# Kernel optimization log

Measured on AMD Instinct MI355X. Metric: run time of the kernel, lower is better.

Reference implementation:

```python
import jax, jax.numpy as jnp
import numpy as np
from jax import lax

N = 2048
P = 256
F_J = 0.05      # sparsity of recurrent matrix J
F_OUT = 0.05    # sparsity of readout
DT = 0.1
ON_TIME = 10
T = 200


def _activation(x):
    # Tanh_shifted_and_scaled: rates in [0, 1]
    return 0.5 * (1.0 + jnp.tanh(x))


def setup_inputs() -> dict:
    key = jax.random.key(0)
    k1, k2, k3, k4, k5 = jax.random.split(key, 5)
    # patterns ~ Uniform(-1, 1), shape [N, P]
    patterns = jax.random.uniform(k1, (N, P), jnp.float32, -1.0, 1.0)
    # sparse recurrent matrix J: gaussian values, density F_J, gain g
    g = 10.0 * 0.1 ** 0.25 / np.sqrt(N * P * np.sqrt(F_J))
    J_dense = jax.random.normal(k2, (N, N), jnp.float32) * jnp.float32(g)
    mask = jax.random.uniform(k3, (N, N)) < F_J
    J = jnp.where(mask, J_dense, 0.0).astype(jnp.float32)
    # sparse readout: ones at a random F_OUT fraction of units (frozen)
    w_out = (jax.random.uniform(k4, (N,)) < F_OUT).astype(jnp.float32)
    return {"patterns": patterns, "J": J, "w_out": w_out, "N_time_steps": T}


def reference(patterns, J, w_out, N_time_steps):
    # Batched over all P patterns at once (columns of [N, P] state).
    n = patterns.shape[0]
    x0 = jnp.zeros_like(patterns)           # [N, P]
    r0 = _activation(x0)

    def step(carry, ti):
        x, rates = carry
        inp = jnp.where(ti < ON_TIME, patterns, 0.0)      # [N, P]
        x = x + DT * (-x + J @ rates + inp)               # [N, P]
        rates = _activation(x)
        out_t = w_out @ rates                             # [P]
        return (x, rates), out_t

    _, outs = lax.scan(step, (x0, r0), jnp.arange(N_time_steps))  # [T, P]
    readout = outs.T / n                                   # [P, T]
    return readout
```

## Files before the change

### kernel.cpp

```cpp
#include <hip/hip_runtime.h>
#include <hip/hip_bf16.h>


#define NN 2048
#define PP 256
#define DT_C 0.1f
#define ON_TIME_C 10

typedef __attribute__((ext_vector_type(8))) short bf16x8;
typedef __attribute__((ext_vector_type(4))) float f32x4;

__device__ __forceinline__ unsigned short bf16rne(float f) {
    unsigned b = __float_as_uint(f);
    return (unsigned short)((b + 0x7FFFu + ((b >> 16) & 1u)) >> 16);
}
__device__ __forceinline__ int kperm(int s) {
    return ((s & 15) >> 2) * 8 + (s & 3) + ((s >> 4) << 2);
}

__global__ void convert_J_kernel(const float* __restrict__ J,
                                 unsigned short* __restrict__ Jp) {
    int i = blockIdx.x * blockDim.x + threadIdx.x;
    int row = i >> 11, k = i & 2047;
    Jp[((size_t)row << 11) + (k & ~31) + kperm(k & 31)] = bf16rne(J[i]);
}

__global__ void init_kernel(float* __restrict__ x,
                            unsigned short* __restrict__ rT,
                            float* __restrict__ out, int nout) {
    int i = blockIdx.x * blockDim.x + threadIdx.x;
    x[i] = 0.0f;
    rT[i] = 0x3F00;
    if (i < nout) out[i] = 0.0f;
}

#define AS1 __attribute__((address_space(1)))
#define AS3 __attribute__((address_space(3)))
#define GLOAD16(g, l) \
    __builtin_amdgcn_global_load_lds((const AS1 void*)(g), (AS3 void*)(l), 16, 0, 0)

__global__ __launch_bounds__(256, 1) void gemm_step_kernel(
    const unsigned short* __restrict__ Jp,
    const unsigned short* __restrict__ rin,
    unsigned short* __restrict__ rout,
    float* __restrict__ x, const float* __restrict__ patterns,
    const float* __restrict__ w_out, float* __restrict__ out,
    int t, int T, int with_input) {

    __shared__ char smem[49152];

    const int tid  = threadIdx.x;
    const int w    = tid >> 6;
    const int lane = tid & 63;
    const int wm   = w >> 1, wn = w & 1;

    const int bid   = (blockIdx.x & 7) * 32 + (blockIdx.x >> 3);
    const int mbase = (bid >> 3) * 64;
    const int nbase = (bid & 7) * 32;

    const int r8 = lane >> 3, p8 = lane & 7;
    const int xr16 = (p8 ^ r8) * 16;
    const char* gA0 = (const char*)Jp  + (((size_t)(mbase + (2*w+0)*8 + r8)) << 12) + xr16;
    const char* gA1 = (const char*)Jp  + (((size_t)(mbase + (2*w+1)*8 + r8)) << 12) + xr16;
    const char* gB  = (const char*)rin + (((size_t)(nbase +  w*8      + r8)) << 12) + xr16;
    const int ldsA0 = (2*w+0) * 1024, ldsA1 = (2*w+1) * 1024, ldsB = 8192 + w * 1024;

    const int cx  = ((lane >> 4) ^ (lane & 7)) * 16;
    const int vA0 = (wm*32      + (lane & 15)) * 128 + cx;
    const int vA1 = (wm*32 + 16 + (lane & 15)) * 128 + cx;
    const int vB  = 8192 + (wn*16 + (lane & 15)) * 128 + cx;

    float xv[2][4], pat[2][4], wsc[2][4];
    #pragma unroll
    for (int mf = 0; mf < 2; ++mf)
        #pragma unroll
        for (int rg = 0; rg < 4; ++rg) {
            int m = mbase + wm*32 + mf*16 + 4*(lane>>4) + rg;
            int n = nbase + wn*16 + (lane & 15);
            size_t o = ((size_t)m << 8) + n;
            xv[mf][rg]  = x[o];
            pat[mf][rg] = with_input ? patterns[o] : 0.0f;
            wsc[mf][rg] = (w_out[m] != 0.0f) ? (1.0f / (float)NN) : 0.0f;
        }

    f32x4 acc[2] = {{0.f,0.f,0.f,0.f}, {0.f,0.f,0.f,0.f}};

    GLOAD16(gA0,       smem + 0*12288 + ldsA0);
    GLOAD16(gA1,       smem + 0*12288 + ldsA1);
    GLOAD16(gB,        smem + 0*12288 + ldsB);
    GLOAD16(gA0 + 128, smem + 1*12288 + ldsA0);
    GLOAD16(gA1 + 128, smem + 1*12288 + ldsA1);
    GLOAD16(gB  + 128, smem + 1*12288 + ldsB);

    #pragma unroll
    for (int ks = 0; ks < 32; ++ks) {
        if (ks < 30) {
            const int bo = ((ks + 2) & 3) * 12288;
            GLOAD16(gA0 + (ks+2)*128, smem + bo + ldsA0);
            GLOAD16(gA1 + (ks+2)*128, smem + bo + ldsA1);
            GLOAD16(gB  + (ks+2)*128, smem + bo + ldsB);
        }
        if (ks < 30)       asm volatile("s_waitcnt vmcnt(6)" ::: "memory");
        else if (ks == 30) asm volatile("s_waitcnt vmcnt(3)" ::: "memory");
        else               asm volatile("s_waitcnt vmcnt(0)" ::: "memory");
        __builtin_amdgcn_s_barrier();
        __builtin_amdgcn_sched_barrier(0);

        const int bb = (ks & 3) * 12288;
        bf16x8 a0  = *(const bf16x8*)(smem + bb + vA0);
        bf16x8 a1  = *(const bf16x8*)(smem + bb + vA1);
        bf16x8 b0  = *(const bf16x8*)(smem + bb + vB);
        bf16x8 a0h = *(const bf16x8*)(smem + bb + (vA0 ^ 64));
        bf16x8 a1h = *(const bf16x8*)(smem + bb + (vA1 ^ 64));
        bf16x8 b0h = *(const bf16x8*)(smem + bb + (vB  ^ 64));
        acc[0] = __builtin_amdgcn_mfma_f32_16x16x32_bf16(a0,  b0,  acc[0], 0, 0, 0);
        acc[1] = __builtin_amdgcn_mfma_f32_16x16x32_bf16(a1,  b0,  acc[1], 0, 0, 0);
        acc[0] = __builtin_amdgcn_mfma_f32_16x16x32_bf16(a0h, b0h, acc[0], 0, 0, 0);
        acc[1] = __builtin_amdgcn_mfma_f32_16x16x32_bf16(a1h, b0h, acc[1], 0, 0, 0);
    }

    __syncthreads();

    #pragma unroll
    for (int mf = 0; mf < 2; ++mf)
        #pragma unroll
        for (int rg = 0; rg < 4; ++rg) {
            float xo = xv[mf][rg];
            float xn = xo + DT_C * (acc[mf][rg] + pat[mf][rg] - xo);
            int m = mbase + wm*32 + mf*16 + 4*(lane>>4) + rg;
            int n = nbase + wn*16 + (lane & 15);
            x[((size_t)m << 8) + n] = xn;
            float r = 0.5f * (1.0f + tanhf(xn));
            if (wsc[mf][rg] != 0.0f)
                atomicAdd(&out[(size_t)n * T + t], r * wsc[mf][rg]);
            int mloc = wm*32 + mf*16 + 4*(lane>>4) + rg;
            int pos  = (mloc & 32) + kperm(mloc & 31);
            int nloc = wn*16 + (lane & 15);
            int byte = nloc*128 + (((pos >> 3) ^ (nloc & 7)) * 16) + (pos & 7)*2;
            *(unsigned short*)(smem + byte) = bf16rne(r);
        }
    __syncthreads();
    {
        int nl = tid >> 3, p = tid & 7;
        uint4 v = *(const uint4*)(smem + nl*128 + ((p ^ (nl & 7)) * 16));
        *(uint4*)((char*)rout + (((size_t)(nbase + nl)) << 12) + mbase*2 + p*16) = v;
    }
}

extern "C" void kernel_launch(void* const* d_in, const int* in_sizes, int n_in,
                              void* d_out, int out_size, void* d_ws, size_t ws_size,
                              hipStream_t stream) {
    const float* patterns = (const float*)d_in[0];
    const float* J        = (const float*)d_in[1];
    const float* w_out    = (const float*)d_in[2];
    float* out            = (float*)d_out;

    int T = out_size / PP;

    size_t off = 0;
    auto alloc = [&](size_t bytes) {
        void* p = (char*)d_ws + off;
        off += (bytes + 255) & ~(size_t)255;
        return p;
    };
    unsigned short* Jp = (unsigned short*)alloc((size_t)NN * NN * 2);
    unsigned short* r0 = (unsigned short*)alloc((size_t)PP * NN * 2);
    unsigned short* r1 = (unsigned short*)alloc((size_t)PP * NN * 2);
    float*          x  = (float*)         alloc((size_t)NN * PP * 4);
    (void)ws_size; (void)n_in; (void)in_sizes;

    convert_J_kernel<<<(NN * NN) / 256, 256, 0, stream>>>(J, Jp);
    init_kernel<<<(NN * PP) / 256, 256, 0, stream>>>(x, r0, out, PP * T);

    for (int t = 0; t < T; ++t) {
        const unsigned short* rin = (t & 1) ? r1 : r0;
        unsigned short*      rout = (t & 1) ? r0 : r1;
        gemm_step_kernel<<<256, 256, 0, stream>>>(Jp, rin, rout, x, patterns,
                                                  w_out, out, t, T,
                                                  (t < ON_TIME_C) ? 1 : 0);
    }
}
```

Baseline: 2.120 ms.

## Use 512-thread blocks with 128-wide K stages and one MFMA tile per wave

Doubles the block to 8 waves, so each wave now computes a single 16x16 output tile instead of two, and doubles the K chunk per pipeline stage to 128 (four MFMAs per stage, half as many barriers). LDS staging grows to 96 KB with a new 16-chunk XOR swizzle. The goal is more waves per CU to hide load latency and fewer barrier round trips per step. In exchange, each wave has fewer MFMAs to cover its LDS reads, and the large LDS footprint caps residency at one block per CU.

```diff
diff --git a/kernel.cpp b/kernel.cpp
--- a/kernel.cpp
+++ b/kernel.cpp
@@ -39,7 +39,7 @@
 #define GLOAD16(g, l) \
     __builtin_amdgcn_global_load_lds((const AS1 void*)(g), (AS3 void*)(l), 16, 0, 0)
 
-__global__ __launch_bounds__(256, 1) void gemm_step_kernel(
+__global__ __launch_bounds__(512, 1) void gemm_step_kernel(
     const unsigned short* __restrict__ Jp,
     const unsigned short* __restrict__ rin,
     unsigned short* __restrict__ rout,
@@ -47,7 +47,7 @@
     const float* __restrict__ w_out, float* __restrict__ out,
     int t, int T, int with_input) {
 
-    __shared__ char smem[49152];
+    __shared__ char smem[98304];
 
     const int tid  = threadIdx.x;
     const int w    = tid >> 6;
@@ -58,92 +58,91 @@
     const int mbase = (bid >> 3) * 64;
     const int nbase = (bid & 7) * 32;
 
-    const int r8 = lane >> 3, p8 = lane & 7;
-    const int xr16 = (p8 ^ r8) * 16;
-    const char* gA0 = (const char*)Jp  + (((size_t)(mbase + (2*w+0)*8 + r8)) << 12) + xr16;
-    const char* gA1 = (const char*)Jp  + (((size_t)(mbase + (2*w+1)*8 + r8)) << 12) + xr16;
-    const char* gB  = (const char*)rin + (((size_t)(nbase +  w*8      + r8)) << 12) + xr16;
-    const int ldsA0 = (2*w+0) * 1024, ldsA1 = (2*w+1) * 1024, ldsB = 8192 + w * 1024;
+    const int rA0 = 8 * w + (lane >> 4);
+    const int rA1 = rA0 + 4;
+    const int rB  = 4 * w + (lane >> 4);
+    const char* gA0 = (const char*)Jp  + (((size_t)(mbase + rA0)) << 12)
+                      + (((lane & 15) ^ (rA0 & 15)) << 4);
+    const char* gA1 = (const char*)Jp  + (((size_t)(mbase + rA1)) << 12)
+                      + (((lane & 15) ^ (rA1 & 15)) << 4);
+    const char* gB  = (const char*)rin + (((size_t)(nbase + rB )) << 12)
+                      + (((lane & 15) ^ (rB  & 15)) << 4);
+    const int ldsA0 = (8 * w)     * 256;
+    const int ldsA1 = (8 * w + 4) * 256;
+    const int ldsB  = 16384 + 4 * w * 256;
 
-    const int cx  = ((lane >> 4) ^ (lane & 7)) * 16;
-    const int vA0 = (wm*32      + (lane & 15)) * 128 + cx;
-    const int vA1 = (wm*32 + 16 + (lane & 15)) * 128 + cx;
-    const int vB  = 8192 + (wn*16 + (lane & 15)) * 128 + cx;
+    const int mr = wm * 16 + (lane & 15);
+    const int nr = wn * 16 + (lane & 15);
 
-    float xv[2][4], pat[2][4], wsc[2][4];
+    float xv[4], pat[4], wsc[4];
     #pragma unroll
-    for (int mf = 0; mf < 2; ++mf)
-        #pragma unroll
-        for (int rg = 0; rg < 4; ++rg) {
-            int m = mbase + wm*32 + mf*16 + 4*(lane>>4) + rg;
-            int n = nbase + wn*16 + (lane & 15);
-            size_t o = ((size_t)m << 8) + n;
-            xv[mf][rg]  = x[o];
-            pat[mf][rg] = with_input ? patterns[o] : 0.0f;
-            wsc[mf][rg] = (w_out[m] != 0.0f) ? (1.0f / (float)NN) : 0.0f;
-        }
+    for (int rg = 0; rg < 4; ++rg) {
+        int m = mbase + wm * 16 + (lane >> 4) * 4 + rg;
+        int n = nbase + wn * 16 + (lane & 15);
+        size_t o = ((size_t)m << 8) + n;
+        xv[rg]  = x[o];
+        pat[rg] = with_input ? patterns[o] : 0.0f;
+        wsc[rg] = (w_out[m] != 0.0f) ? (1.0f / (float)NN) : 0.0f;
+    }
 
-    f32x4 acc[2] = {{0.f,0.f,0.f,0.f}, {0.f,0.f,0.f,0.f}};
+    f32x4 acc = {0.f, 0.f, 0.f, 0.f};
 
-    GLOAD16(gA0,       smem + 0*12288 + ldsA0);
-    GLOAD16(gA1,       smem + 0*12288 + ldsA1);
-    GLOAD16(gB,        smem + 0*12288 + ldsB);
-    GLOAD16(gA0 + 128, smem + 1*12288 + ldsA0);
-    GLOAD16(gA1 + 128, smem + 1*12288 + ldsA1);
-    GLOAD16(gB  + 128, smem + 1*12288 + ldsB);
+    GLOAD16(gA0,       smem + 0 * 24576 + ldsA0);
+    GLOAD16(gA1,       smem + 0 * 24576 + ldsA1);
+    GLOAD16(gB,        smem + 0 * 24576 + ldsB);
+    GLOAD16(gA0 + 256, smem + 1 * 24576 + ldsA0);
+    GLOAD16(gA1 + 256, smem + 1 * 24576 + ldsA1);
+    GLOAD16(gB  + 256, smem + 1 * 24576 + ldsB);
 
     #pragma unroll
-    for (int ks = 0; ks < 32; ++ks) {
-        if (ks < 30) {
-            const int bo = ((ks + 2) & 3) * 12288;
-            GLOAD16(gA0 + (ks+2)*128, smem + bo + ldsA0);
-            GLOAD16(gA1 + (ks+2)*128, smem + bo + ldsA1);
-            GLOAD16(gB  + (ks+2)*128, smem + bo + ldsB);
+    for (int ph = 0; ph < 16; ++ph) {
+        if (ph < 14) {
+            const int bo = ((ph + 2) & 3) * 24576;
+            GLOAD16(gA0 + (ph + 2) * 256, smem + bo + ldsA0);
+            GLOAD16(gA1 + (ph + 2) * 256, smem + bo + ldsA1);
+            GLOAD16(gB  + (ph + 2) * 256, smem + bo + ldsB);
         }
-        if (ks < 30)       asm volatile("s_waitcnt vmcnt(6)" ::: "memory");
-        else if (ks == 30) asm volatile("s_waitcnt vmcnt(3)" ::: "memory");
+        if (ph < 14)       asm volatile("s_waitcnt vmcnt(6)" ::: "memory");
+        else if (ph == 14) asm volatile("s_waitcnt vmcnt(3)" ::: "memory");
         else               asm volatile("s_waitcnt vmcnt(0)" ::: "memory");
         __builtin_amdgcn_s_barrier();
         __builtin_amdgcn_sched_barrier(0);
 
-        const int bb = (ks & 3) * 12288;
-        bf16x8 a0  = *(const bf16x8*)(smem + bb + vA0);
-        bf16x8 a1  = *(const bf16x8*)(smem + bb + vA1);
-        bf16x8 b0  = *(const bf16x8*)(smem + bb + vB);
-        bf16x8 a0h = *(const bf16x8*)(smem + bb + (vA0 ^ 64));
-        bf16x8 a1h = *(const bf16x8*)(smem + bb + (vA1 ^ 64));
-        bf16x8 b0h = *(const bf16x8*)(smem + bb + (vB  ^ 64));
-        acc[0] = __builtin_amdgcn_mfma_f32_16x16x32_bf16(a0,  b0,  acc[0], 0, 0, 0);
-        acc[1] = __builtin_amdgcn_mfma_f32_16x16x32_bf16(a1,  b0,  acc[1], 0, 0, 0);
-        acc[0] = __builtin_amdgcn_mfma_f32_16x16x32_bf16(a0h, b0h, acc[0], 0, 0, 0);
-        acc[1] = __builtin_amdgcn_mfma_f32_16x16x32_bf16(a1h, b0h, acc[1], 0, 0, 0);
+        const int bb = (ph & 3) * 24576;
+        bf16x8 a[4], b[4];
+        #pragma unroll
+        for (int g = 0; g < 4; ++g) {
+            int c = g * 4 + (lane >> 4);
+            a[g] = *(const bf16x8*)(smem + bb + mr * 256 + ((c ^ (mr & 15)) << 4));
+            b[g] = *(const bf16x8*)(smem + bb + 16384 + nr * 256 + ((c ^ (nr & 15)) << 4));
+        }
+        #pragma unroll
+        for (int g = 0; g < 4; ++g)
+            acc = __builtin_amdgcn_mfma_f32_16x16x32_bf16(a[g], b[g], acc, 0, 0, 0);
     }
 
     __syncthreads();
 
     #pragma unroll
-    for (int mf = 0; mf < 2; ++mf)
-        #pragma unroll
-        for (int rg = 0; rg < 4; ++rg) {
-            float xo = xv[mf][rg];
-            float xn = xo + DT_C * (acc[mf][rg] + pat[mf][rg] - xo);
-            int m = mbase + wm*32 + mf*16 + 4*(lane>>4) + rg;
-            int n = nbase + wn*16 + (lane & 15);
-            x[((size_t)m << 8) + n] = xn;
-            float r = 0.5f * (1.0f + tanhf(xn));
-            if (wsc[mf][rg] != 0.0f)
-                atomicAdd(&out[(size_t)n * T + t], r * wsc[mf][rg]);
-            int mloc = wm*32 + mf*16 + 4*(lane>>4) + rg;
-            int pos  = (mloc & 32) + kperm(mloc & 31);
-            int nloc = wn*16 + (lane & 15);
-            int byte = nloc*128 + (((pos >> 3) ^ (nloc & 7)) * 16) + (pos & 7)*2;
-            *(unsigned short*)(smem + byte) = bf16rne(r);
-        }
+    for (int rg = 0; rg < 4; ++rg) {
+        float xo = xv[rg];
+        float xn = xo + DT_C * (acc[rg] + pat[rg] - xo);
+        int mloc = wm * 16 + (lane >> 4) * 4 + rg;
+        int nloc = wn * 16 + (lane & 15);
+        int m = mbase + mloc, n = nbase + nloc;
+        x[((size_t)m << 8) + n] = xn;
+        float r = 0.5f * (1.0f + tanhf(xn));
+        if (wsc[rg] != 0.0f)
+            atomicAdd(&out[(size_t)n * T + t], r * wsc[rg]);
+        int pos  = (mloc & ~31) + kperm(mloc & 31);
+        int byte = nloc * 128 + (((pos >> 3) ^ (nloc & 7)) << 4) + (pos & 7) * 2;
+        *(unsigned short*)(smem + byte) = bf16rne(r);
+    }
     __syncthreads();
-    {
+    if (tid < 256) {
         int nl = tid >> 3, p = tid & 7;
-        uint4 v = *(const uint4*)(smem + nl*128 + ((p ^ (nl & 7)) * 16));
-        *(uint4*)((char*)rout + (((size_t)(nbase + nl)) << 12) + mbase*2 + p*16) = v;
+        uint4 v = *(const uint4*)(smem + nl * 128 + ((p ^ (nl & 7)) << 4));
+        *(uint4*)((char*)rout + (((size_t)(nbase + nl)) << 12) + mbase * 2 + p * 16) = v;
     }
 }
 
@@ -175,7 +174,7 @@
     for (int t = 0; t < T; ++t) {
         const unsigned short* rin = (t & 1) ? r1 : r0;
         unsigned short*      rout = (t & 1) ? r0 : r1;
-        gemm_step_kernel<<<256, 256, 0, stream>>>(Jp, rin, rout, x, patterns,
+        gemm_step_kernel<<<256, 512, 0, stream>>>(Jp, rin, rout, x, patterns,
                                                   w_out, out, t, T,
                                                   (t < ON_TIME_C) ? 1 : 0);
     }
```

Result: faster. 1.972 ms (-7.0%).
